# Kernel optimization log

Hardware: AMD Instinct MI355X
Metric: run time of the kernel (lower is better)

The kernel has to match this reference:

```python
import jax, jax.numpy as jnp
import numpy as np

N = 100000
E = 1600000
BN_EPS = 1e-5
L2_EPS = 1e-12


def _sage_conv(x, src, dst, wl, bl, wr):
    # mean-aggregate source features onto destination nodes
    s = jax.ops.segment_sum(x[src], dst, num_segments=N)          # [N, C]
    cnt = jax.ops.segment_sum(jnp.ones((E,), x.dtype), dst, num_segments=N)
    agg = s / jnp.maximum(cnt, 1.0)[:, None]
    out = agg @ wl.T + bl + x @ wr.T                              # lin_l(agg) + lin_r(x)
    # normalize=True -> row-wise L2 normalization
    nrm = jnp.sqrt(jnp.sum(out * out, axis=-1, keepdims=True))
    return out / jnp.maximum(nrm, L2_EPS)


def _bn(x, g, b):
    # BatchNorm1d, training-mode batch statistics (biased variance)
    m = jnp.mean(x, axis=0)
    v = jnp.mean((x - m) ** 2, axis=0)
    return (x - m) / jnp.sqrt(v + BN_EPS) * g + b


def setup_inputs() -> dict:
    key = jax.random.key(0)
    ks = jax.random.split(key, 24)
    dims = [(4, 6), (6, 8), (8, 16), (16, 32)]
    inp = {
        "x": jax.random.normal(ks[0], (N, 4), jnp.float32),
        "edge_index": jax.random.randint(ks[1], (2, E), 0, N, dtype=jnp.int64),
    }
    ki = 2
    for li, (ci, co) in enumerate(dims, start=1):
        sc = 1.0 / np.sqrt(ci)
        inp[f"w{li}l"] = jax.random.uniform(ks[ki], (co, ci), jnp.float32, -sc, sc); ki += 1
        inp[f"b{li}l"] = jax.random.uniform(ks[ki], (co,), jnp.float32, -sc, sc); ki += 1
        inp[f"w{li}r"] = jax.random.uniform(ks[ki], (co, ci), jnp.float32, -sc, sc); ki += 1
    for li, co in enumerate([6, 8, 16], start=1):
        inp[f"g{li}"] = jnp.ones((co,), jnp.float32)
        inp[f"be{li}"] = jnp.zeros((co,), jnp.float32)
    return inp


def reference(x, edge_index,
              w1l, b1l, w1r, w2l, b2l, w2r, w3l, b3l, w3r, w4l, b4l, w4r,
              g1, be1, g2, be2, g3, be3):
    src, dst = edge_index[0], edge_index[1]
    h = _sage_conv(x, src, dst, w1l, b1l, w1r)
    h = _bn(jax.nn.relu(h), g1, be1)
    h = _sage_conv(h, src, dst, w2l, b2l, w2r)
    h = _bn(jax.nn.relu(h), g2, be2)
    h = _sage_conv(h, src, dst, w3l, b3l, w3r)
    h = _bn(jax.nn.relu(h), g3, be3)
    h = _sage_conv(h, src, dst, w4l, b4l, w4r)
    return jax.nn.relu(h)
```

## Files before the change

kernel.cpp:

```cpp
#include <hip/hip_runtime.h>

#define NNODES 100000
#define NEDGES 1600000
#define BN_EPS 1e-5f
#define L2_EPS 1e-12f

#define BKT_SHIFT 9
#define BKT_SIZE  512
#define NBKT      196
#define CHUNK     4096
#define NBLK_E    391

__global__ void hist_kernel(const int* __restrict__ dst,
                            int* __restrict__ blk_hist, float* __restrict__ stats) {
    __shared__ int h[NBKT];
    for (int i = threadIdx.x; i < NBKT; i += blockDim.x) h[i] = 0;
    if (blockIdx.x == 0 && threadIdx.x < 128) {
        stats[threadIdx.x] = 0.0f;
        stats[threadIdx.x + 128] = 0.0f;
        stats[threadIdx.x + 256] = 0.0f;
    }
    __syncthreads();
    int base = blockIdx.x * CHUNK;
    int end  = min(base + CHUNK, NEDGES);
    for (int e = base + threadIdx.x; e < end; e += blockDim.x)
        atomicAdd(&h[dst[e] >> BKT_SHIFT], 1);
    __syncthreads();
    for (int i = threadIdx.x; i < NBKT; i += blockDim.x)
        blk_hist[blockIdx.x * NBKT + i] = h[i];
}

__global__ void scan_blocks(const int* __restrict__ blk_hist,
                            int* __restrict__ blk_off, int* __restrict__ bucket_total) {
    __shared__ int tmp[512];
    int b = blockIdx.x;
    int i = threadIdx.x;
    int v = (i < NBLK_E) ? blk_hist[i * NBKT + b] : 0;
    tmp[i] = v;
    __syncthreads();
    for (int off = 1; off < 512; off <<= 1) {
        int t = (i >= off) ? tmp[i - off] : 0;
        __syncthreads();
        tmp[i] += t;
        __syncthreads();
    }
    if (i < NBLK_E) blk_off[i * NBKT + b] = tmp[i] - v;
    if (i == 511) bucket_total[b] = tmp[511];
}

__global__ void scan_buckets(const int* __restrict__ bucket_total, int* __restrict__ bucket_base) {
    __shared__ int tmp[256];
    int v = (threadIdx.x < NBKT) ? bucket_total[threadIdx.x] : 0;
    tmp[threadIdx.x] = v;
    __syncthreads();
    for (int off = 1; off < 256; off <<= 1) {
        int t = (threadIdx.x >= off) ? tmp[threadIdx.x - off] : 0;
        __syncthreads();
        tmp[threadIdx.x] += t;
        __syncthreads();
    }
    if (threadIdx.x < NBKT) bucket_base[threadIdx.x] = tmp[threadIdx.x] - v;
    if (threadIdx.x == 0) bucket_base[NBKT] = NEDGES;
}

__global__ void bucket_scatter(const int* __restrict__ src, const int* __restrict__ dst,
                               const int* __restrict__ blk_off, const int* __restrict__ bucket_base,
                               unsigned int* __restrict__ staged) {
    __shared__ int cur[NBKT];
    for (int i = threadIdx.x; i < NBKT; i += blockDim.x)
        cur[i] = blk_off[blockIdx.x * NBKT + i] + bucket_base[i];
    __syncthreads();
    int base = blockIdx.x * CHUNK;
    int end  = min(base + CHUNK, NEDGES);
    for (int e = base + threadIdx.x; e < end; e += blockDim.x) {
        int d = dst[e];
        int b = d >> BKT_SHIFT;
        int p = atomicAdd(&cur[b], 1);
        staged[p] = ((unsigned)(d & (BKT_SIZE - 1)) << 23) | (unsigned)src[e];
    }
}

__global__ void csr_finalize(const unsigned int* __restrict__ staged,
                             const int* __restrict__ bucket_base,
                             int* __restrict__ row_ptr, int* __restrict__ col) {
    __shared__ int nh[BKT_SIZE];
    __shared__ int cur[BKT_SIZE];
    int b = blockIdx.x;
    int beg = bucket_base[b], end = bucket_base[b + 1];

    nh[threadIdx.x] = 0;
    __syncthreads();
    for (int e = beg + threadIdx.x; e < end; e += blockDim.x)
        atomicAdd(&nh[staged[e] >> 23], 1);
    __syncthreads();

    int v = nh[threadIdx.x];
    cur[threadIdx.x] = v;
    __syncthreads();
    for (int off = 1; off < 512; off <<= 1) {
        int t = (threadIdx.x >= off) ? cur[threadIdx.x - off] : 0;
        __syncthreads();
        cur[threadIdx.x] += t;
        __syncthreads();
    }
    int excl = cur[threadIdx.x] - v;

    int node = b * BKT_SIZE + threadIdx.x;
    if (node < NNODES) row_ptr[node] = beg + excl;
    if (b == 0 && threadIdx.x == 0) row_ptr[NNODES] = NEDGES;
    __syncthreads();
    cur[threadIdx.x] = excl;
    __syncthreads();

    for (int e = beg + threadIdx.x; e < end; e += blockDim.x) {
        unsigned pk = staged[e];
        int l = (int)(pk >> 23);
        int p = atomicAdd(&cur[l], 1);
        col[beg + p] = (int)(pk & 0x7FFFFF);
    }
}

template<int CI>
__device__ __forceinline__ void load_row(const float* __restrict__ p, float* r) {
    constexpr int N4 = CI / 4;
#pragma unroll
    for (int i = 0; i < N4; i++) {
        float4 v = ((const float4*)p)[i];
        r[4*i] = v.x; r[4*i+1] = v.y; r[4*i+2] = v.z; r[4*i+3] = v.w;
    }
    if constexpr ((CI % 4) >= 2) {
        float2 v = ((const float2*)(p + 4 * N4))[0];
        r[4*N4] = v.x; r[4*N4+1] = v.y;
    }
    if constexpr ((CI % 2) == 1) r[CI - 1] = p[CI - 1];
}

template<int CI, int SI, int CO, int SO, int G, bool IN_AFFINE, bool DO_STATS>
__global__ void layer_kernel(const int* __restrict__ row_ptr, const int* __restrict__ col,
                             const float* __restrict__ h,
                             const float* __restrict__ ssum_in, const float* __restrict__ ssq_in,
                             const float* __restrict__ g_in, const float* __restrict__ b_in,
                             const float* __restrict__ wl, const float* __restrict__ bl,
                             const float* __restrict__ wr,
                             float* __restrict__ y,
                             float* __restrict__ stat_sum, float* __restrict__ stat_sq) {
    constexpr int NPB = 256 / G;
    constexpr int OPL = (CO + G - 1) / G;
    constexpr int PCI = CI + 1;

    __shared__ float sWl[CO * PCI];
    __shared__ float sWr[CO * PCI];
    __shared__ float sBl[CO];
    __shared__ float sSc[CI];
    __shared__ float sSh[CI];
    __shared__ float red_sum[CO];
    __shared__ float red_sq[CO];

    for (int i = threadIdx.x; i < CO * CI; i += blockDim.x) {
        int o = i / CI, c = i - o * CI;
        sWl[o * PCI + c] = wl[i];
        sWr[o * PCI + c] = wr[i];
    }
    if (threadIdx.x < CO) {
        sBl[threadIdx.x] = bl[threadIdx.x];
        if (DO_STATS) { red_sum[threadIdx.x] = 0.0f; red_sq[threadIdx.x] = 0.0f; }
    }
    if (IN_AFFINE && threadIdx.x < CI) {
        float m  = ssum_in[threadIdx.x] * (1.0f / NNODES);
        float vv = ssq_in[threadIdx.x] * (1.0f / NNODES) - m * m;
        float s  = g_in[threadIdx.x] / sqrtf(vv + BN_EPS);
        sSc[threadIdx.x] = s;
        sSh[threadIdx.x] = b_in[threadIdx.x] - m * s;
    }
    __syncthreads();

    int node = blockIdx.x * NPB + (threadIdx.x / G);
    int g    = threadIdx.x & (G - 1);
    bool valid = node < NNODES;

    float acc[CI];
#pragma unroll
    for (int c = 0; c < CI; c++) acc[c] = 0.0f;

    int beg = 0, end = 0;
    if (valid) {
        beg = row_ptr[node];
        end = row_ptr[node + 1];
        int j = beg + g;
        for (; j + 3 * G < end; j += 4 * G) {
            int i0 = col[j], i1 = col[j + G], i2 = col[j + 2 * G], i3 = col[j + 3 * G];
            float r0[CI], r1[CI], r2[CI], r3[CI];
            load_row<CI>(h + (long)i0 * SI, r0);
            load_row<CI>(h + (long)i1 * SI, r1);
            load_row<CI>(h + (long)i2 * SI, r2);
            load_row<CI>(h + (long)i3 * SI, r3);
#pragma unroll
            for (int c = 0; c < CI; c++) acc[c] += (r0[c] + r1[c]) + (r2[c] + r3[c]);
        }
        for (; j + G < end; j += 2 * G) {
            int i0 = col[j], i1 = col[j + G];
            float r0[CI], r1[CI];
            load_row<CI>(h + (long)i0 * SI, r0);
            load_row<CI>(h + (long)i1 * SI, r1);
#pragma unroll
            for (int c = 0; c < CI; c++) acc[c] += r0[c] + r1[c];
        }
        if (j < end) {
            float r0[CI];
            load_row<CI>(h + (long)col[j] * SI, r0);
#pragma unroll
            for (int c = 0; c < CI; c++) acc[c] += r0[c];
        }
    }

#pragma unroll
    for (int m = 1; m < G; m <<= 1)
#pragma unroll
        for (int c = 0; c < CI; c++) acc[c] += __shfl_xor(acc[c], m);

    float out[OPL];
    float nrm2 = 0.0f;
    if (valid) {
        float ic = 1.0f / fmaxf((float)(end - beg), 1.0f);
        float xin[CI];
        load_row<CI>(h + (long)node * SI, xin);
        float agg[CI];
#pragma unroll
        for (int c = 0; c < CI; c++) {
            float a  = acc[c] * ic;
            float xv = xin[c];
            if (IN_AFFINE) {
                a  = a  * sSc[c] + sSh[c];
                xv = xv * sSc[c] + sSh[c];
            }
            agg[c] = a;
            xin[c] = xv;
        }
#pragma unroll
        for (int k = 0; k < OPL; k++) {
            int o = g * OPL + k;
            float v = 0.0f;
            if (o < CO) {
                v = sBl[o];
#pragma unroll
                for (int c = 0; c < CI; c++)
                    v += sWl[o * PCI + c] * agg[c] + sWr[o * PCI + c] * xin[c];
            }
            out[k] = v;
            nrm2 += v * v;
        }
    }
#pragma unroll
    for (int m = 1; m < G; m <<= 1) nrm2 += __shfl_xor(nrm2, m);

    if (valid) {
        float inv_nrm = 1.0f / fmaxf(sqrtf(nrm2), L2_EPS);
#pragma unroll
        for (int k = 0; k < OPL; k++) {
            int o = g * OPL + k;
            if (o < CO) {
                float v = fmaxf(out[k] * inv_nrm, 0.0f);
                y[(long)node * SO + o] = v;
                if (DO_STATS) {
                    atomicAdd(&red_sum[o], v);
                    atomicAdd(&red_sq[o], v * v);
                }
            }
        }
    }

    if (DO_STATS) {
        __syncthreads();
        if (threadIdx.x < CO) {
            atomicAdd(&stat_sum[threadIdx.x], red_sum[threadIdx.x]);
            atomicAdd(&stat_sq[threadIdx.x], red_sq[threadIdx.x]);
        }
    }
}

extern "C" void kernel_launch(void* const* d_in, const int* in_sizes, int n_in,
                              void* d_out, int out_size, void* d_ws, size_t ws_size,
                              hipStream_t stream) {
    const float* x   = (const float*)d_in[0];
    const int*   ei  = (const int*)d_in[1];
    const int*   src = ei;
    const int*   dst = ei + NEDGES;

    const float* w1l = (const float*)d_in[2];
    const float* b1l = (const float*)d_in[3];
    const float* w1r = (const float*)d_in[4];
    const float* w2l = (const float*)d_in[5];
    const float* b2l = (const float*)d_in[6];
    const float* w2r = (const float*)d_in[7];
    const float* w3l = (const float*)d_in[8];
    const float* b3l = (const float*)d_in[9];
    const float* w3r = (const float*)d_in[10];
    const float* w4l = (const float*)d_in[11];
    const float* b4l = (const float*)d_in[12];
    const float* w4r = (const float*)d_in[13];
    const float* g1  = (const float*)d_in[14];
    const float* be1 = (const float*)d_in[15];
    const float* g2  = (const float*)d_in[16];
    const float* be2 = (const float*)d_in[17];
    const float* g3  = (const float*)d_in[18];
    const float* be3 = (const float*)d_in[19];

    char* w = (char*)d_ws;
    int* blk_hist     = (int*)w;  w += NBLK_E * NBKT * 4;
    int* blk_off      = (int*)w;  w += NBLK_E * NBKT * 4;
    int* bucket_total = (int*)w;  w += 256 * 4;
    int* bucket_base  = (int*)w;  w += 256 * 4;
    int* row_ptr      = (int*)w;  w += (NNODES + 8) * 4;
    int* col          = (int*)w;  w += NEDGES * 4;
    float* hA         = (float*)w; w += NNODES * 16 * 4;
    float* hB         = (float*)w; w += NNODES * 16 * 4;
    float* stats      = (float*)w; w += 3 * 128 * 4;
    unsigned int* staged = (unsigned int*)hB;

    float* ssum1 = stats + 0 * 128, *ssq1 = ssum1 + 32;
    float* ssum2 = stats + 1 * 128, *ssq2 = ssum2 + 32;
    float* ssum3 = stats + 2 * 128, *ssq3 = ssum3 + 32;

    hist_kernel   <<<NBLK_E, 256, 0, stream>>>(dst, blk_hist, stats);
    scan_blocks   <<<NBKT, 512, 0, stream>>>(blk_hist, blk_off, bucket_total);
    scan_buckets  <<<1, 256, 0, stream>>>(bucket_total, bucket_base);
    bucket_scatter<<<NBLK_E, 256, 0, stream>>>(src, dst, blk_off, bucket_base, staged);
    csr_finalize  <<<NBKT, 512, 0, stream>>>(staged, bucket_base, row_ptr, col);

    layer_kernel<4, 4, 6, 8, 4, false, true><<<(NNODES * 4 + 255) / 256, 256, 0, stream>>>(
        row_ptr, col, x, nullptr, nullptr, nullptr, nullptr,
        w1l, b1l, w1r, hA, ssum1, ssq1);

    layer_kernel<6, 8, 8, 8, 4, true, true><<<(NNODES * 4 + 255) / 256, 256, 0, stream>>>(
        row_ptr, col, hA, ssum1, ssq1, g1, be1,
        w2l, b2l, w2r, hB, ssum2, ssq2);

    layer_kernel<8, 8, 16, 16, 4, true, true><<<(NNODES * 4 + 255) / 256, 256, 0, stream>>>(
        row_ptr, col, hB, ssum2, ssq2, g2, be2,
        w3l, b3l, w3r, hA, ssum3, ssq3);

    layer_kernel<16, 16, 32, 32, 8, true, false><<<(NNODES * 8 + 255) / 256, 256, 0, stream>>>(
        row_ptr, col, hA, ssum3, ssq3, g3, be3,
        w4l, b4l, w4r, (float*)d_out, nullptr, nullptr);
}
```

Baseline: 273.5 us.

## Rework CSR build: wavefront-shuffle scans, vectorized edge loads, fewer larger blocks

Replaces the shared-memory Hillis-Steele scans in the CSR construction kernels with a wavefront-shuffle block exclusive scan. The histogram and bucket-scatter kernels now read edges as int4 and run in 196 blocks of 512 threads over 8192-edge chunks. The per-block histogram is stored transposed so the block scan reads it contiguously. The aim is to cut barrier count and load instructions in the preprocessing stage, at the cost of fewer blocks, which may hurt occupancy and raise shared-atomic contention per block.

```diff
diff --git a/kernel.cpp b/kernel.cpp
--- a/kernel.cpp
+++ b/kernel.cpp
@@ -8,11 +8,38 @@
 #define BKT_SHIFT 9
 #define BKT_SIZE  512
 #define NBKT      196
-#define CHUNK     4096
-#define NBLK_E    391
+#define CHUNK     8192
+#define NBLK_E    196
+
+template<int NT>
+__device__ __forceinline__ int block_excl_scan(int v, int* wsum) {
+    __syncthreads();
+    constexpr int NW = NT / 64;
+    int incl = v;
+#pragma unroll
+    for (int off = 1; off < 64; off <<= 1) {
+        int t = __shfl_up(incl, off);
+        if ((threadIdx.x & 63) >= off) incl += t;
+    }
+    int wid = threadIdx.x >> 6;
+    if ((threadIdx.x & 63) == 63) wsum[wid] = incl;
+    __syncthreads();
+    if (threadIdx.x < NW) {
+        int w = wsum[threadIdx.x];
+#pragma unroll
+        for (int off = 1; off < NW; off <<= 1) {
+            int t = __shfl_up(w, off);
+            if ((int)threadIdx.x >= off) w += t;
+        }
+        wsum[threadIdx.x] = w;
+    }
+    __syncthreads();
+    int base = wid ? wsum[wid - 1] : 0;
+    return base + incl - v;
+}
 
 __global__ void hist_kernel(const int* __restrict__ dst,
-                            int* __restrict__ blk_hist, float* __restrict__ stats) {
+                            int* __restrict__ blk_hist_T, float* __restrict__ stats) {
     __shared__ int h[NBKT];
     for (int i = threadIdx.x; i < NBKT; i += blockDim.x) h[i] = 0;
     if (blockIdx.x == 0 && threadIdx.x < 128) {
@@ -23,44 +50,36 @@
     __syncthreads();
     int base = blockIdx.x * CHUNK;
     int end  = min(base + CHUNK, NEDGES);
-    for (int e = base + threadIdx.x; e < end; e += blockDim.x)
-        atomicAdd(&h[dst[e] >> BKT_SHIFT], 1);
+    for (int e = base + threadIdx.x * 4; e < end; e += blockDim.x * 4) {
+        int4 d = *reinterpret_cast<const int4*>(dst + e);
+        atomicAdd(&h[d.x >> BKT_SHIFT], 1);
+        atomicAdd(&h[d.y >> BKT_SHIFT], 1);
+        atomicAdd(&h[d.z >> BKT_SHIFT], 1);
+        atomicAdd(&h[d.w >> BKT_SHIFT], 1);
+    }
     __syncthreads();
     for (int i = threadIdx.x; i < NBKT; i += blockDim.x)
-        blk_hist[blockIdx.x * NBKT + i] = h[i];
-}
-
-__global__ void scan_blocks(const int* __restrict__ blk_hist,
+        blk_hist_T[i * NBLK_E + blockIdx.x] = h[i];
+}
+
+__global__ void scan_blocks(const int* __restrict__ blk_hist_T,
                             int* __restrict__ blk_off, int* __restrict__ bucket_total) {
-    __shared__ int tmp[512];
+    __shared__ int wsum[4];
     int b = blockIdx.x;
     int i = threadIdx.x;
-    int v = (i < NBLK_E) ? blk_hist[i * NBKT + b] : 0;
-    tmp[i] = v;
-    __syncthreads();
-    for (int off = 1; off < 512; off <<= 1) {
-        int t = (i >= off) ? tmp[i - off] : 0;
-        __syncthreads();
-        tmp[i] += t;
-        __syncthreads();
-    }
-    if (i < NBLK_E) blk_off[i * NBKT + b] = tmp[i] - v;
-    if (i == 511) bucket_total[b] = tmp[511];
+    int v = (i < NBLK_E) ? blk_hist_T[b * NBLK_E + i] : 0;
+    int excl = block_excl_scan<256>(v, wsum);
+    if (i < NBLK_E) blk_off[i * NBKT + b] = excl;
+    if (i == 255) bucket_total[b] = excl + v;
 }
 
 __global__ void scan_buckets(const int* __restrict__ bucket_total, int* __restrict__ bucket_base) {
-    __shared__ int tmp[256];
-    int v = (threadIdx.x < NBKT) ? bucket_total[threadIdx.x] : 0;
-    tmp[threadIdx.x] = v;
-    __syncthreads();
-    for (int off = 1; off < 256; off <<= 1) {
-        int t = (threadIdx.x >= off) ? tmp[threadIdx.x - off] : 0;
-        __syncthreads();
-        tmp[threadIdx.x] += t;
-        __syncthreads();
-    }
-    if (threadIdx.x < NBKT) bucket_base[threadIdx.x] = tmp[threadIdx.x] - v;
-    if (threadIdx.x == 0) bucket_base[NBKT] = NEDGES;
+    __shared__ int wsum[4];
+    int i = threadIdx.x;
+    int v = (i < NBKT) ? bucket_total[i] : 0;
+    int excl = block_excl_scan<256>(v, wsum);
+    if (i < NBKT) bucket_base[i] = excl;
+    if (i == 255) bucket_base[NBKT] = excl + v;
 }
 
 __global__ void bucket_scatter(const int* __restrict__ src, const int* __restrict__ dst,
@@ -72,11 +91,17 @@
     __syncthreads();
     int base = blockIdx.x * CHUNK;
     int end  = min(base + CHUNK, NEDGES);
-    for (int e = base + threadIdx.x; e < end; e += blockDim.x) {
-        int d = dst[e];
-        int b = d >> BKT_SHIFT;
-        int p = atomicAdd(&cur[b], 1);
-        staged[p] = ((unsigned)(d & (BKT_SIZE - 1)) << 23) | (unsigned)src[e];
+    for (int e = base + threadIdx.x * 4; e < end; e += blockDim.x * 4) {
+        int4 d = *reinterpret_cast<const int4*>(dst + e);
+        int4 s = *reinterpret_cast<const int4*>(src + e);
+        int p0 = atomicAdd(&cur[d.x >> BKT_SHIFT], 1);
+        staged[p0] = ((unsigned)(d.x & (BKT_SIZE - 1)) << 23) | (unsigned)s.x;
+        int p1 = atomicAdd(&cur[d.y >> BKT_SHIFT], 1);
+        staged[p1] = ((unsigned)(d.y & (BKT_SIZE - 1)) << 23) | (unsigned)s.y;
+        int p2 = atomicAdd(&cur[d.z >> BKT_SHIFT], 1);
+        staged[p2] = ((unsigned)(d.z & (BKT_SIZE - 1)) << 23) | (unsigned)s.z;
+        int p3 = atomicAdd(&cur[d.w >> BKT_SHIFT], 1);
+        staged[p3] = ((unsigned)(d.w & (BKT_SIZE - 1)) << 23) | (unsigned)s.w;
     }
 }
 
@@ -85,6 +110,7 @@
                              int* __restrict__ row_ptr, int* __restrict__ col) {
     __shared__ int nh[BKT_SIZE];
     __shared__ int cur[BKT_SIZE];
+    __shared__ int wsum[8];
     int b = blockIdx.x;
     int beg = bucket_base[b], end = bucket_base[b + 1];
 
@@ -95,20 +121,11 @@
     __syncthreads();
 
     int v = nh[threadIdx.x];
-    cur[threadIdx.x] = v;
-    __syncthreads();
-    for (int off = 1; off < 512; off <<= 1) {
-        int t = (threadIdx.x >= off) ? cur[threadIdx.x - off] : 0;
-        __syncthreads();
-        cur[threadIdx.x] += t;
-        __syncthreads();
-    }
-    int excl = cur[threadIdx.x] - v;
+    int excl = block_excl_scan<512>(v, wsum);
 
     int node = b * BKT_SIZE + threadIdx.x;
     if (node < NNODES) row_ptr[node] = beg + excl;
     if (b == 0 && threadIdx.x == 0) row_ptr[NNODES] = NEDGES;
-    __syncthreads();
     cur[threadIdx.x] = excl;
     __syncthreads();
 
@@ -321,10 +338,10 @@
     float* ssum2 = stats + 1 * 128, *ssq2 = ssum2 + 32;
     float* ssum3 = stats + 2 * 128, *ssq3 = ssum3 + 32;
 
-    hist_kernel   <<<NBLK_E, 256, 0, stream>>>(dst, blk_hist, stats);
-    scan_blocks   <<<NBKT, 512, 0, stream>>>(blk_hist, blk_off, bucket_total);
+    hist_kernel   <<<NBLK_E, 512, 0, stream>>>(dst, blk_hist, stats);
+    scan_blocks   <<<NBKT, 256, 0, stream>>>(blk_hist, blk_off, bucket_total);
     scan_buckets  <<<1, 256, 0, stream>>>(bucket_total, bucket_base);
-    bucket_scatter<<<NBLK_E, 256, 0, stream>>>(src, dst, blk_off, bucket_base, staged);
+    bucket_scatter<<<NBLK_E, 512, 0, stream>>>(src, dst, blk_off, bucket_base, staged);
     csr_finalize  <<<NBKT, 512, 0, stream>>>(staged, bucket_base, row_ptr, col);
 
     layer_kernel<4, 4, 6, 8, 4, false, true><<<(NNODES * 4 + 255) / 256, 256, 0, stream>>>(
```

New measurement: 292.1 us. 1.07x slower.
